# Performance work log

Hardware: AMD Instinct MI355X
Metric: run time of the kernel (lower is better)

Reference implementation:

```python
import jax, jax.numpy as jnp
import numpy as np

N = 524288
E = 16          # embedding_dim
R = 128         # dense grid resolution
H = 128         # hidden_dim
W0_SIREN = 30.0


def trilinear(grid, p):
    """grid: [R,R,R,E]; p: [N,3] in [0,1]. Returns [N,E]."""
    r = grid.shape[0]
    x = p * (r - 1)
    i0 = jnp.clip(jnp.floor(x), 0, r - 2).astype(jnp.int32)   # [N,3]
    f = x - i0.astype(x.dtype)                                # [N,3] fractional
    gf = grid.reshape(-1, grid.shape[-1])                     # [R^3, E]
    out = jnp.zeros((p.shape[0], grid.shape[-1]), dtype=grid.dtype)
    for dx in (0, 1):
        wx = f[:, 0] if dx else (1.0 - f[:, 0])
        for dy in (0, 1):
            wy = f[:, 1] if dy else (1.0 - f[:, 1])
            for dz in (0, 1):
                wz = f[:, 2] if dz else (1.0 - f[:, 2])
                idx = (i0[:, 0] + dx) * r * r + (i0[:, 1] + dy) * r + (i0[:, 2] + dz)
                out = out + gf[idx] * (wx * wy * wz)[:, None]
    return out


def siren(h, W0, b0, W1, b1, Wo, bo):
    h = jnp.sin(W0_SIREN * (h @ W0.T + b0))
    h = jnp.sin(W0_SIREN * (h @ W1.T + b1))
    return h @ Wo.T + bo   # [N,1]


def setup_inputs() -> dict:
    key = jax.random.key(0)
    ks = jax.random.split(key, 8)
    positions = jax.random.uniform(ks[0], (N, 3), dtype=jnp.float32)  # in [0,1)
    grid = jax.random.uniform(ks[1], (R, R, R, E), jnp.float32, -1e-4, 1e-4)
    din = E + 3
    c0 = float(np.sqrt(6.0 / din) / W0_SIREN)
    c1 = float(np.sqrt(6.0 / H) / W0_SIREN)
    W0 = jax.random.uniform(ks[2], (H, din), jnp.float32, -c0, c0)
    b0 = jax.random.uniform(ks[3], (H,), jnp.float32, -c0, c0)
    W1 = jax.random.uniform(ks[4], (H, H), jnp.float32, -c1, c1)
    b1 = jax.random.uniform(ks[5], (H,), jnp.float32, -c1, c1)
    Wo = jax.random.uniform(ks[6], (1, H), jnp.float32, -c1, c1)
    bo = jax.random.uniform(ks[7], (1,), jnp.float32, -c1, c1)
    return {"positions": positions, "grid": grid, "W0": W0, "b0": b0,
            "W1": W1, "b1": b1, "Wo": Wo, "bo": bo}


def reference(positions, grid, W0, b0, W1, b1, Wo, bo):
    # torch code rebinds positions = positions*0.5+0.5 BEFORE autograd.grad,
    # so the eikonal gradient is w.r.t. the transformed coordinates p.
    p = positions * 0.5 + 0.5

    def sdf_fn(pp):
        emb = trilinear(grid, pp)
        return siren(jnp.concatenate([emb, pp], axis=-1), W0, b0, W1, b1, Wo, bo)

    sdf, vjp_fn = jax.vjp(sdf_fn, p)
    (grad_x,) = vjp_fn(jnp.ones_like(sdf))
    return sdf, grad_x
```

## Files before the change

kernel.cpp:

```cpp
#include <hip/hip_runtime.h>
#include <math.h>

#define NPTS 524288
#define EDIM 16
#define RES  128
#define HDIM 128
#define DIN  19
#define OXs  (RES*RES*EDIM)
#define OYs  (RES*EDIM)
#define OZs  (EDIM)
#define NBLK 256
#define NWAVE 12
#define BATCH (NWAVE * 16)
#define NITER 11

typedef _Float16 f16;
typedef __attribute__((ext_vector_type(8))) _Float16 f16x8;
typedef __attribute__((ext_vector_type(4))) float f32x4;

#define WS_P1 0
#define WS_P2 32768
#define WS_P0 65536
#define WS_P3 73728
#define WS_T  81920
#define WS_BYTES 84992

__global__ void pack_weights(const float* __restrict__ W0, const float* __restrict__ b0,
                             const float* __restrict__ W1, const float* __restrict__ b1,
                             const float* __restrict__ Wo, unsigned char* __restrict__ ws) {
    int idx = blockIdx.x * 256 + threadIdx.x;
    f16* p1 = (f16*)(ws + WS_P1);
    f16* p2 = (f16*)(ws + WS_P2);
    f16* p0 = (f16*)(ws + WS_P0);
    f16* p3 = (f16*)(ws + WS_P3);
    float* tb = (float*)(ws + WS_T);
    if (idx < 16384) {
        int e = idx & 7, l = (idx >> 3) & 63, t = (idx >> 9) & 3, nt = idx >> 11;
        int c = l & 15, g = l >> 4;
        p1[idx] = (f16)W1[(c + 16*nt)*HDIM + (8*g + e + 32*t)];
    } else if (idx < 32768) {
        int i = idx - 16384;
        int e = i & 7, l = (i >> 3) & 63, t = (i >> 9) & 3, nt = i >> 11;
        int c = l & 15, g = l >> 4;
        p2[i] = (f16)W1[(8*g + e + 32*t)*HDIM + (c + 16*nt)];
    } else if (idx < 36864) {
        int i = idx - 32768;
        int e = i & 7, l = (i >> 3) & 63, nt = i >> 9;
        int c = l & 15, g = l >> 4;
        int d = 8*g + e;
        p0[i] = (d < EDIM) ? (f16)W0[(c + 16*nt)*DIN + d] : (f16)0.f;
    } else if (idx < 40960) {
        int i = idx - 36864;
        int e = i & 7, l = (i >> 3) & 63, t = (i >> 9) & 3, nt = i >> 11;
        int c = l & 15, g = l >> 4;
        int din = c + 16*nt;
        p3[i] = (din < DIN) ? (f16)W0[(8*g + e + 32*t)*DIN + din] : (f16)0.f;
    } else if (idx < 41728) {
        int i = idx - 40960;
        int j = i & 127, sel = i >> 7;
        float v;
        if (sel == 0)      v = W0[j*DIN + 16];
        else if (sel == 1) v = W0[j*DIN + 17];
        else if (sel == 2) v = W0[j*DIN + 18];
        else if (sel == 3) v = b0[j];
        else if (sel == 4) v = b1[j];
        else               v = Wo[j];
        tb[i] = v;
    }
}

__global__ __launch_bounds__(768, 1)
void sdf_mfma(const float* __restrict__ pos,
              const float* __restrict__ gridp,
              const unsigned char* __restrict__ ws,
              const float* __restrict__ bo,
              float* __restrict__ out) {
    __shared__ f16 sP1[16384];
    __shared__ f16 sP2[16384];
    __shared__ f16 sP0[4096];
    __shared__ f16 sP3[4096];
    __shared__ float sT[768];
    __shared__ unsigned char sBounce[NWAVE][4352];

    const int tid = threadIdx.x;
    {
        const uint4* src = (const uint4*)ws;
        uint4* d1 = (uint4*)sP1;
        uint4* d2 = (uint4*)sP2;
        uint4* d0 = (uint4*)sP0;
        uint4* d3 = (uint4*)sP3;
        uint4* dt = (uint4*)sT;
#pragma unroll
        for (int i = 0; i < 3; ++i) {
            int k = tid + i * 768;
            if (k < 2048) { d1[k] = src[k]; d2[k] = src[2048 + k]; }
        }
        if (tid < 512) { d0[tid] = src[4096 + tid]; d3[tid] = src[4608 + tid]; }
        if (tid < 192) dt[tid] = src[5120 + tid];
    }
    __syncthreads();

    const int l = tid & 63, w = tid >> 6;
    const int c = l & 15, g = l >> 4;

    f16* sBW = (f16*)sBounce[w];
    const f16x8* P0 = (const f16x8*)sP0;
    const f16x8* P1 = (const f16x8*)sP1;
    const f16x8* P2 = (const f16x8*)sP2;
    const f16x8* P3 = (const f16x8*)sP3;
    const f32x4 z4 = {0.f, 0.f, 0.f, 0.f};
    const float bov = bo[0];

#pragma unroll 1
    for (int it = 0; it < NITER; ++it) {
        const int pbase = (blockIdx.x * NITER + it) * BATCH + w * 16;
        if (pbase >= NPTS) continue;
        const int pt = pbase + c;

        const float px = fmaf(pos[3*pt+0], 0.5f, 0.5f);
        const float py = fmaf(pos[3*pt+1], 0.5f, 0.5f);
        const float pz = fmaf(pos[3*pt+2], 0.5f, 0.5f);
        const float x0 = px*127.f, x1 = py*127.f, x2 = pz*127.f;
        int i0 = (int)floorf(x0); i0 = i0 < 0 ? 0 : (i0 > 126 ? 126 : i0);
        int i1 = (int)floorf(x1); i1 = i1 < 0 ? 0 : (i1 > 126 ? 126 : i1);
        int i2 = (int)floorf(x2); i2 = i2 < 0 ? 0 : (i2 > 126 ? 126 : i2);
        const float f0 = x0 - (float)i0, f1 = x1 - (float)i1, f2 = x2 - (float)i2;
        const float wx1 = f0, wx0 = 1.f - f0;
        const float wy1 = f1, wy0 = 1.f - f1;
        const float wz1 = f2, wz0 = 1.f - f2;
        const float* gb = gridp + (size_t)((i0*RES + i1)*RES + i2)*EDIM;

        float w8[8] = {0.f,0.f,0.f,0.f,0.f,0.f,0.f,0.f};
        if (g < 2) {
#pragma unroll
            for (int cr = 0; cr < 8; ++cr) {
                const float* gp = gb + ((cr>>2)&1)*OXs + ((cr>>1)&1)*OYs + (cr&1)*OZs + 8*g;
                float4 qa = *(const float4*)gp;
                float4 qb = *(const float4*)(gp + 4);
                const float wc = ((cr&4)?wx1:wx0) * ((cr&2)?wy1:wy0) * ((cr&1)?wz1:wz0);
                w8[0] = fmaf(wc, qa.x, w8[0]);  w8[1] = fmaf(wc, qa.y, w8[1]);
                w8[2] = fmaf(wc, qa.z, w8[2]);  w8[3] = fmaf(wc, qa.w, w8[3]);
                w8[4] = fmaf(wc, qb.x, w8[4]);  w8[5] = fmaf(wc, qb.y, w8[5]);
                w8[6] = fmaf(wc, qb.z, w8[6]);  w8[7] = fmaf(wc, qb.w, w8[7]);
            }
        }
        f16x8 afe;
#pragma unroll
        for (int m = 0; m < 8; ++m) afe[m] = (f16)w8[m];

        f32x4 acc[8];
#pragma unroll
        for (int nt = 0; nt < 8; ++nt)
            acc[nt] = __builtin_amdgcn_mfma_f32_16x16x32_f16(afe, P0[nt*64 + l], z4, 0, 0, 0);

        float rpx[4], rpy[4], rpz[4];
#pragma unroll
        for (int r = 0; r < 4; ++r) {
            const int pr = pbase + 4*g + r;
            rpx[r] = fmaf(pos[3*pr+0], 0.5f, 0.5f);
            rpy[r] = fmaf(pos[3*pr+1], 0.5f, 0.5f);
            rpz[r] = fmaf(pos[3*pr+2], 0.5f, 0.5f);
        }
        float t0a[8][4];
#pragma unroll
        for (int nt = 0; nt < 8; ++nt) {
            const int j = c + 16*nt;
            const float t16 = sT[j], t17 = sT[128+j], t18 = sT[256+j], tb0 = sT[384+j];
#pragma unroll
            for (int r = 0; r < 4; ++r) {
                float a0 = acc[nt][r] + tb0;
                a0 = fmaf(rpx[r], t16, a0);
                a0 = fmaf(rpy[r], t17, a0);
                a0 = fmaf(rpz[r], t18, a0);
                const float t0 = 30.f * a0;
                t0a[nt][r] = t0;
                sBW[(4*g + r)*136 + j] = (f16)__sinf(t0);
            }
        }
        asm volatile("s_waitcnt lgkmcnt(0)" ::: "memory");

        f16x8 af[4];
#pragma unroll
        for (int t = 0; t < 4; ++t)
            af[t] = *(const f16x8*)&sBW[c*136 + 32*t + 8*g];
#pragma unroll
        for (int nt = 0; nt < 8; ++nt) {
            f32x4 a = z4;
#pragma unroll
            for (int t = 0; t < 4; ++t)
                a = __builtin_amdgcn_mfma_f32_16x16x32_f16(af[t], P1[(nt*4+t)*64 + l], a, 0, 0, 0);
            acc[nt] = a;
        }

        float sp[4] = {0.f, 0.f, 0.f, 0.f};
#pragma unroll
        for (int nt = 0; nt < 8; ++nt) {
            const int j = c + 16*nt;
            const float b1j = sT[512+j], woj = sT[640+j];
#pragma unroll
            for (int r = 0; r < 4; ++r) {
                const float t1 = 30.f * (acc[nt][r] + b1j);
                sp[r] = fmaf(woj, __sinf(t1), sp[r]);
                sBW[(4*g + r)*136 + j] = (f16)(30.f * woj * __cosf(t1));
            }
        }
#pragma unroll
        for (int r = 0; r < 4; ++r) {
            sp[r] += __shfl_xor(sp[r], 1);
            sp[r] += __shfl_xor(sp[r], 2);
            sp[r] += __shfl_xor(sp[r], 4);
            sp[r] += __shfl_xor(sp[r], 8);
        }
        if (c == 0) {
#pragma unroll
            for (int r = 0; r < 4; ++r) out[pbase + 4*g + r] = sp[r] + bov;
        }
        asm volatile("s_waitcnt lgkmcnt(0)" ::: "memory");

        float4 ca[2][4];
#pragma unroll
        for (int h = 0; h < 2; ++h) {
            const int cr = 2*g + h;
            const float* gp = gb + ((cr>>2)&1)*OXs + ((cr>>1)&1)*OYs + (cr&1)*OZs;
            ca[h][0] = *(const float4*)gp;
            ca[h][1] = *(const float4*)(gp + 4);
            ca[h][2] = *(const float4*)(gp + 8);
            ca[h][3] = *(const float4*)(gp + 12);
        }

#pragma unroll
        for (int t = 0; t < 4; ++t)
            af[t] = *(const f16x8*)&sBW[c*136 + 32*t + 8*g];
#pragma unroll
        for (int nt = 0; nt < 8; ++nt) {
            f32x4 a = z4;
#pragma unroll
            for (int t = 0; t < 4; ++t)
                a = __builtin_amdgcn_mfma_f32_16x16x32_f16(af[t], P2[(nt*4+t)*64 + l], a, 0, 0, 0);
            acc[nt] = a;
        }

#pragma unroll
        for (int nt = 0; nt < 8; ++nt) {
            const int k = c + 16*nt;
#pragma unroll
            for (int r = 0; r < 4; ++r) {
                const float da0 = acc[nt][r] * (30.f * __cosf(t0a[nt][r]));
                sBW[(4*g + r)*136 + k] = (f16)da0;
            }
        }
        asm volatile("s_waitcnt lgkmcnt(0)" ::: "memory");

#pragma unroll
        for (int t = 0; t < 4; ++t)
            af[t] = *(const f16x8*)&sBW[c*136 + 32*t + 8*g];
        f32x4 d3a = z4, d3b = z4;
#pragma unroll
        for (int t = 0; t < 4; ++t) {
            d3a = __builtin_amdgcn_mfma_f32_16x16x32_f16(af[t], P3[t*64 + l],     d3a, 0, 0, 0);
            d3b = __builtin_amdgcn_mfma_f32_16x16x32_f16(af[t], P3[(4+t)*64 + l], d3b, 0, 0, 0);
        }

        float* sDV = (float*)sBounce[w];
#pragma unroll
        for (int r = 0; r < 4; ++r) sDV[(4*g + r)*20 + c] = d3a[r];
        if (c < 3) {
#pragma unroll
            for (int r = 0; r < 4; ++r) sDV[(4*g + r)*20 + 16 + c] = d3b[r];
        }
        asm volatile("s_waitcnt lgkmcnt(0)" ::: "memory");

        const f32x4 dva = *(const f32x4*)&sDV[c*20 + 0];
        const f32x4 dvb = *(const f32x4*)&sDV[c*20 + 4];
        const f32x4 dvc = *(const f32x4*)&sDV[c*20 + 8];
        const f32x4 dvd = *(const f32x4*)&sDV[c*20 + 12];
        float scv[2];
#pragma unroll
        for (int h = 0; h < 2; ++h) {
            float s = ca[h][0].x*dva[0] + ca[h][0].y*dva[1] + ca[h][0].z*dva[2] + ca[h][0].w*dva[3]
                    + ca[h][1].x*dvb[0] + ca[h][1].y*dvb[1] + ca[h][1].z*dvb[2] + ca[h][1].w*dvb[3]
                    + ca[h][2].x*dvc[0] + ca[h][2].y*dvc[1] + ca[h][2].z*dvc[2] + ca[h][2].w*dvc[3]
                    + ca[h][3].x*dvd[0] + ca[h][3].y*dvd[1] + ca[h][3].z*dvd[2] + ca[h][3].w*dvd[3];
            scv[h] = s;
        }
        float* sSC = (float*)sBounce[w] + 320;
        sSC[c*8 + 2*g]     = scv[0];
        sSC[c*8 + 2*g + 1] = scv[1];
        asm volatile("s_waitcnt lgkmcnt(0)" ::: "memory");
        if (g == 0) {
            const float* scp = &sSC[c*8];
            const float sc0 = scp[0], sc1 = scp[1], sc2 = scp[2], sc3 = scp[3];
            const float sc4 = scp[4], sc5 = scp[5], sc6 = scp[6], sc7 = scp[7];
            const float gx = 127.f * (wy0*wz0*(sc4-sc0) + wy0*wz1*(sc5-sc1) +
                                      wy1*wz0*(sc6-sc2) + wy1*wz1*(sc7-sc3));
            const float gy = 127.f * (wx0*wz0*(sc2-sc0) + wx0*wz1*(sc3-sc1) +
                                      wx1*wz0*(sc6-sc4) + wx1*wz1*(sc7-sc5));
            const float gz = 127.f * (wx0*wy0*(sc1-sc0) + wx0*wy1*(sc3-sc2) +
                                      wx1*wy0*(sc5-sc4) + wx1*wy1*(sc7-sc6));
            out[NPTS + 3*pt + 0] = gx + sDV[c*20 + 16];
            out[NPTS + 3*pt + 1] = gy + sDV[c*20 + 17];
            out[NPTS + 3*pt + 2] = gz + sDV[c*20 + 18];
        }
    }
}

#define JCHUNK 64
__global__ void transpose_w1(const float* __restrict__ W1, float* __restrict__ W1T) {
    int idx = blockIdx.x * 256 + threadIdx.x;
    if (idx < HDIM * HDIM) {
        int j = idx >> 7, k = idx & 127;
        W1T[k * HDIM + j] = W1[j * HDIM + k];
    }
}
#define LOAD16(gq)                                   \
    float4 q0 = *(const float4*)((gq) + 0);          \
    float4 q1 = *(const float4*)((gq) + 4);          \
    float4 q2 = *(const float4*)((gq) + 8);          \
    float4 q3 = *(const float4*)((gq) + 12);

template<int RS, int CS>
__global__ __launch_bounds__(256, 2)
void sdf_fused(const float* __restrict__ pos, const float* __restrict__ gridp,
               const float* __restrict__ W0, const float* __restrict__ b0,
               const float* __restrict__ W1m, const float* __restrict__ b1,
               const float* __restrict__ Wo, const float* __restrict__ bo,
               float* __restrict__ out) {
    const int i = blockIdx.x * 256 + threadIdx.x;
    if (i >= NPTS) return;
    const float W0S = 30.0f;
    const float px = fmaf(pos[3*i+0], 0.5f, 0.5f);
    const float py = fmaf(pos[3*i+1], 0.5f, 0.5f);
    const float pz = fmaf(pos[3*i+2], 0.5f, 0.5f);
    const float x0 = px*127.f, x1 = py*127.f, x2 = pz*127.f;
    int i0 = (int)floorf(x0); i0 = i0 < 0 ? 0 : (i0 > 126 ? 126 : i0);
    int i1 = (int)floorf(x1); i1 = i1 < 0 ? 0 : (i1 > 126 ? 126 : i1);
    int i2 = (int)floorf(x2); i2 = i2 < 0 ? 0 : (i2 > 126 ? 126 : i2);
    const float f0 = x0-(float)i0, f1 = x1-(float)i1, f2 = x2-(float)i2;
    const float wx1 = f0, wx0 = 1.f-f0, wy1 = f1, wy0 = 1.f-f1, wz1 = f2, wz0 = 1.f-f2;
    const float* gb = gridp + (size_t)((i0*RES+i1)*RES+i2)*EDIM;
    float cw[8];
    cw[0]=wx0*wy0*wz0; cw[1]=wx0*wy0*wz1; cw[2]=wx0*wy1*wz0; cw[3]=wx0*wy1*wz1;
    cw[4]=wx1*wy0*wz0; cw[5]=wx1*wy0*wz1; cw[6]=wx1*wy1*wz0; cw[7]=wx1*wy1*wz1;
    float v[DIN];
#pragma unroll
    for (int e = 0; e < EDIM; ++e) v[e] = 0.f;
#pragma unroll
    for (int cr = 0; cr < 8; ++cr) {
        const float* gq = gb + ((cr>>2)&1)*OXs + ((cr>>1)&1)*OYs + (cr&1)*OZs;
        LOAD16(gq);
        const float wc = cw[cr];
        v[0]=fmaf(wc,q0.x,v[0]); v[1]=fmaf(wc,q0.y,v[1]); v[2]=fmaf(wc,q0.z,v[2]); v[3]=fmaf(wc,q0.w,v[3]);
        v[4]=fmaf(wc,q1.x,v[4]); v[5]=fmaf(wc,q1.y,v[5]); v[6]=fmaf(wc,q1.z,v[6]); v[7]=fmaf(wc,q1.w,v[7]);
        v[8]=fmaf(wc,q2.x,v[8]); v[9]=fmaf(wc,q2.y,v[9]); v[10]=fmaf(wc,q2.z,v[10]); v[11]=fmaf(wc,q2.w,v[11]);
        v[12]=fmaf(wc,q3.x,v[12]); v[13]=fmaf(wc,q3.y,v[13]); v[14]=fmaf(wc,q3.z,v[14]); v[15]=fmaf(wc,q3.w,v[15]);
    }
    v[16]=px; v[17]=py; v[18]=pz;
    float dv[DIN];
#pragma unroll
    for (int m = 0; m < DIN; ++m) dv[m] = 0.f;
    float sdf = bo[0];
#pragma unroll 1
    for (int cch = 0; cch < HDIM/JCHUNK; ++cch) {
        const int j0 = cch * JCHUNK;
        float a1c[JCHUNK];
#pragma unroll
        for (int jj = 0; jj < JCHUNK; ++jj) a1c[jj] = 0.f;
#pragma unroll 1
        for (int k = 0; k < HDIM; ++k) {
            float a0 = b0[k];
            const float* w0r = W0 + k*DIN;
#pragma unroll
            for (int m = 0; m < DIN; ++m) a0 = fmaf(w0r[m], v[m], a0);
            const float h1 = __sinf(W0S*a0);
            const float* wr = W1m + k*RS + j0*CS;
#pragma unroll
            for (int jj = 0; jj < JCHUNK; ++jj) a1c[jj] = fmaf(wr[jj*CS], h1, a1c[jj]);
        }
#pragma unroll
        for (int jj = 0; jj < JCHUNK; ++jj) {
            const float t = W0S*(a1c[jj] + b1[j0+jj]);
            float s, co; __sincosf(t, &s, &co);
            const float wo = Wo[j0+jj];
            sdf = fmaf(wo, s, sdf);
            a1c[jj] = (W0S*wo)*co;
        }
#pragma unroll 1
        for (int k = 0; k < HDIM; ++k) {
            const float* wr = W1m + k*RS + j0*CS;
            float s0=0.f,s1=0.f,s2=0.f,s3=0.f;
#pragma unroll
            for (int jj = 0; jj < JCHUNK; jj += 4) {
                s0 = fmaf(wr[(jj+0)*CS], a1c[jj+0], s0);
                s1 = fmaf(wr[(jj+1)*CS], a1c[jj+1], s1);
                s2 = fmaf(wr[(jj+2)*CS], a1c[jj+2], s2);
                s3 = fmaf(wr[(jj+3)*CS], a1c[jj+3], s3);
            }
            const float dh1 = (s0+s1)+(s2+s3);
            float a0 = b0[k];
            const float* w0r = W0 + k*DIN;
#pragma unroll
            for (int m = 0; m < DIN; ++m) a0 = fmaf(w0r[m], v[m], a0);
            const float da0 = dh1 * W0S * __cosf(W0S*a0);
#pragma unroll
            for (int m = 0; m < DIN; ++m) dv[m] = fmaf(w0r[m], da0, dv[m]);
        }
    }
    float sc[8];
#pragma unroll
    for (int cr = 0; cr < 8; ++cr) {
        const float* gq = gb + ((cr>>2)&1)*OXs + ((cr>>1)&1)*OYs + (cr&1)*OZs;
        LOAD16(gq);
        float t0 = q0.x*dv[0]+q0.y*dv[1]+q0.z*dv[2]+q0.w*dv[3];
        float t1 = q1.x*dv[4]+q1.y*dv[5]+q1.z*dv[6]+q1.w*dv[7];
        float t2 = q2.x*dv[8]+q2.y*dv[9]+q2.z*dv[10]+q2.w*dv[11];
        float t3 = q3.x*dv[12]+q3.y*dv[13]+q3.z*dv[14]+q3.w*dv[15];
        sc[cr] = (t0+t1)+(t2+t3);
    }
    const float gx = 127.f*(wy0*wz0*(sc[4]-sc[0]) + wy0*wz1*(sc[5]-sc[1]) + wy1*wz0*(sc[6]-sc[2]) + wy1*wz1*(sc[7]-sc[3]));
    const float gy = 127.f*(wx0*wz0*(sc[2]-sc[0]) + wx0*wz1*(sc[3]-sc[1]) + wx1*wz0*(sc[6]-sc[4]) + wx1*wz1*(sc[7]-sc[5]));
    const float gz = 127.f*(wx0*wy0*(sc[1]-sc[0]) + wx0*wy1*(sc[3]-sc[2]) + wx1*wy0*(sc[5]-sc[4]) + wx1*wy1*(sc[7]-sc[6]));
    out[i] = sdf;
    out[NPTS + 3*i + 0] = gx + dv[16];
    out[NPTS + 3*i + 1] = gy + dv[17];
    out[NPTS + 3*i + 2] = gz + dv[18];
}

extern "C" void kernel_launch(void* const* d_in, const int* in_sizes, int n_in,
                              void* d_out, int out_size, void* d_ws, size_t ws_size,
                              hipStream_t stream) {
    const float* pos  = (const float*)d_in[0];
    const float* grid = (const float*)d_in[1];
    const float* W0   = (const float*)d_in[2];
    const float* b0   = (const float*)d_in[3];
    const float* W1   = (const float*)d_in[4];
    const float* b1   = (const float*)d_in[5];
    const float* Wo   = (const float*)d_in[6];
    const float* bo   = (const float*)d_in[7];
    float* out = (float*)d_out;

    if (ws_size >= (size_t)WS_BYTES) {
        pack_weights<<<(41728 + 255)/256, 256, 0, stream>>>(W0, b0, W1, b1, Wo, (unsigned char*)d_ws);
        sdf_mfma<<<NBLK, 768, 0, stream>>>(pos, grid, (const unsigned char*)d_ws, bo, out);
    } else if (ws_size >= (size_t)(HDIM*HDIM*sizeof(float))) {
        float* W1T = (float*)d_ws;
        transpose_w1<<<(HDIM*HDIM + 255)/256, 256, 0, stream>>>(W1, W1T);
        sdf_fused<HDIM, 1><<<NPTS/256, 256, 0, stream>>>(pos, grid, W0, b0, W1T, b1, Wo, bo, out);
    } else {
        sdf_fused<1, HDIM><<<NPTS/256, 256, 0, stream>>>(pos, grid, W0, b0, W1, b1, Wo, bo, out);
    }
}
```

Baseline: 115.6 us.

## Hold small MFMA B operands in registers, split gather across lanes, raise MFMA priority

The P0 and P3 weight fragments now stay in VGPRs per wave instead of LDS, which removes LDS reads from the first and last matmuls and shrinks shared memory. The trilinear embedding gather is spread over all four lane groups: each handles one x-side of the cell and partial sums are combined with a cross-half shuffle, so the gather is no longer confined to half the wave. MFMA sections are wrapped in s_setprio to favour matrix issue across waves. These changes raise register pressure and add a shuffle, which could cause spills at 768 threads.

```diff
diff --git a/kernel.cpp b/kernel.cpp
--- a/kernel.cpp
+++ b/kernel.cpp
@@ -77,8 +77,6 @@
               float* __restrict__ out) {
     __shared__ f16 sP1[16384];
     __shared__ f16 sP2[16384];
-    __shared__ f16 sP0[4096];
-    __shared__ f16 sP3[4096];
     __shared__ float sT[768];
     __shared__ unsigned char sBounce[NWAVE][4352];
 
@@ -87,29 +85,35 @@
         const uint4* src = (const uint4*)ws;
         uint4* d1 = (uint4*)sP1;
         uint4* d2 = (uint4*)sP2;
-        uint4* d0 = (uint4*)sP0;
-        uint4* d3 = (uint4*)sP3;
         uint4* dt = (uint4*)sT;
 #pragma unroll
         for (int i = 0; i < 3; ++i) {
             int k = tid + i * 768;
             if (k < 2048) { d1[k] = src[k]; d2[k] = src[2048 + k]; }
         }
-        if (tid < 512) { d0[tid] = src[4096 + tid]; d3[tid] = src[4608 + tid]; }
         if (tid < 192) dt[tid] = src[5120 + tid];
     }
-    __syncthreads();
 
     const int l = tid & 63, w = tid >> 6;
     const int c = l & 15, g = l >> 4;
 
+    f16x8 B0r[8], B3r[8];
+    {
+        const f16x8* P0g = (const f16x8*)(ws + WS_P0);
+        const f16x8* P3g = (const f16x8*)(ws + WS_P3);
+#pragma unroll
+        for (int nt = 0; nt < 8; ++nt) B0r[nt] = P0g[nt*64 + l];
+#pragma unroll
+        for (int t = 0; t < 8; ++t)  B3r[t] = P3g[t*64 + l];
+    }
+    __syncthreads();
+
     f16* sBW = (f16*)sBounce[w];
-    const f16x8* P0 = (const f16x8*)sP0;
     const f16x8* P1 = (const f16x8*)sP1;
     const f16x8* P2 = (const f16x8*)sP2;
-    const f16x8* P3 = (const f16x8*)sP3;
     const f32x4 z4 = {0.f, 0.f, 0.f, 0.f};
     const float bov = bo[0];
+    const int s = g & 1, q = g >> 1;
 
 #pragma unroll 1
     for (int it = 0; it < NITER; ++it) {
@@ -131,13 +135,14 @@
         const float* gb = gridp + (size_t)((i0*RES + i1)*RES + i2)*EDIM;
 
         float w8[8] = {0.f,0.f,0.f,0.f,0.f,0.f,0.f,0.f};
-        if (g < 2) {
-#pragma unroll
-            for (int cr = 0; cr < 8; ++cr) {
-                const float* gp = gb + ((cr>>2)&1)*OXs + ((cr>>1)&1)*OYs + (cr&1)*OZs + 8*g;
+        {
+            const float wxq = q ? wx1 : wx0;
+#pragma unroll
+            for (int j = 0; j < 4; ++j) {
+                const float* gp = gb + q*OXs + ((j>>1)&1)*OYs + (j&1)*OZs + 8*s;
                 float4 qa = *(const float4*)gp;
                 float4 qb = *(const float4*)(gp + 4);
-                const float wc = ((cr&4)?wx1:wx0) * ((cr&2)?wy1:wy0) * ((cr&1)?wz1:wz0);
+                const float wc = wxq * ((j&2)?wy1:wy0) * ((j&1)?wz1:wz0);
                 w8[0] = fmaf(wc, qa.x, w8[0]);  w8[1] = fmaf(wc, qa.y, w8[1]);
                 w8[2] = fmaf(wc, qa.z, w8[2]);  w8[3] = fmaf(wc, qa.w, w8[3]);
                 w8[4] = fmaf(wc, qb.x, w8[4]);  w8[5] = fmaf(wc, qb.y, w8[5]);
@@ -146,12 +151,17 @@
         }
         f16x8 afe;
 #pragma unroll
-        for (int m = 0; m < 8; ++m) afe[m] = (f16)w8[m];
+        for (int m = 0; m < 8; ++m) {
+            const float full = w8[m] + __shfl_xor(w8[m], 32);
+            afe[m] = (g < 2) ? (f16)full : (f16)0.f;
+        }
 
         f32x4 acc[8];
+        __builtin_amdgcn_s_setprio(1);
 #pragma unroll
         for (int nt = 0; nt < 8; ++nt)
-            acc[nt] = __builtin_amdgcn_mfma_f32_16x16x32_f16(afe, P0[nt*64 + l], z4, 0, 0, 0);
+            acc[nt] = __builtin_amdgcn_mfma_f32_16x16x32_f16(afe, B0r[nt], z4, 0, 0, 0);
+        __builtin_amdgcn_s_setprio(0);
 
         float rpx[4], rpy[4], rpz[4];
 #pragma unroll
@@ -183,6 +193,7 @@
 #pragma unroll
         for (int t = 0; t < 4; ++t)
             af[t] = *(const f16x8*)&sBW[c*136 + 32*t + 8*g];
+        __builtin_amdgcn_s_setprio(1);
 #pragma unroll
         for (int nt = 0; nt < 8; ++nt) {
             f32x4 a = z4;
@@ -191,6 +202,7 @@
                 a = __builtin_amdgcn_mfma_f32_16x16x32_f16(af[t], P1[(nt*4+t)*64 + l], a, 0, 0, 0);
             acc[nt] = a;
         }
+        __builtin_amdgcn_s_setprio(0);
 
         float sp[4] = {0.f, 0.f, 0.f, 0.f};
 #pragma unroll
@@ -231,6 +243,7 @@
 #pragma unroll
         for (int t = 0; t < 4; ++t)
             af[t] = *(const f16x8*)&sBW[c*136 + 32*t + 8*g];
+        __builtin_amdgcn_s_setprio(1);
 #pragma unroll
         for (int nt = 0; nt < 8; ++nt) {
             f32x4 a = z4;
@@ -239,6 +252,7 @@
                 a = __builtin_amdgcn_mfma_f32_16x16x32_f16(af[t], P2[(nt*4+t)*64 + l], a, 0, 0, 0);
             acc[nt] = a;
         }
+        __builtin_amdgcn_s_setprio(0);
 
 #pragma unroll
         for (int nt = 0; nt < 8; ++nt) {
@@ -255,11 +269,13 @@
         for (int t = 0; t < 4; ++t)
             af[t] = *(const f16x8*)&sBW[c*136 + 32*t + 8*g];
         f32x4 d3a = z4, d3b = z4;
+        __builtin_amdgcn_s_setprio(1);
 #pragma unroll
         for (int t = 0; t < 4; ++t) {
-            d3a = __builtin_amdgcn_mfma_f32_16x16x32_f16(af[t], P3[t*64 + l],     d3a, 0, 0, 0);
-            d3b = __builtin_amdgcn_mfma_f32_16x16x32_f16(af[t], P3[(4+t)*64 + l], d3b, 0, 0, 0);
-        }
+            d3a = __builtin_amdgcn_mfma_f32_16x16x32_f16(af[t], B3r[t],     d3a, 0, 0, 0);
+            d3b = __builtin_amdgcn_mfma_f32_16x16x32_f16(af[t], B3r[4 + t], d3b, 0, 0, 0);
+        }
+        __builtin_amdgcn_s_setprio(0);
 
         float* sDV = (float*)sBounce[w];
 #pragma unroll
@@ -277,11 +293,11 @@
         float scv[2];
 #pragma unroll
         for (int h = 0; h < 2; ++h) {
-            float s = ca[h][0].x*dva[0] + ca[h][0].y*dva[1] + ca[h][0].z*dva[2] + ca[h][0].w*dva[3]
-                    + ca[h][1].x*dvb[0] + ca[h][1].y*dvb[1] + ca[h][1].z*dvb[2] + ca[h][1].w*dvb[3]
-                    + ca[h][2].x*dvc[0] + ca[h][2].y*dvc[1] + ca[h][2].z*dvc[2] + ca[h][2].w*dvc[3]
-                    + ca[h][3].x*dvd[0] + ca[h][3].y*dvd[1] + ca[h][3].z*dvd[2] + ca[h][3].w*dvd[3];
-            scv[h] = s;
+            float sdot = ca[h][0].x*dva[0] + ca[h][0].y*dva[1] + ca[h][0].z*dva[2] + ca[h][0].w*dva[3]
+                       + ca[h][1].x*dvb[0] + ca[h][1].y*dvb[1] + ca[h][1].z*dvb[2] + ca[h][1].w*dvb[3]
+                       + ca[h][2].x*dvc[0] + ca[h][2].y*dvc[1] + ca[h][2].z*dvc[2] + ca[h][2].w*dvc[3]
+                       + ca[h][3].x*dvd[0] + ca[h][3].y*dvd[1] + ca[h][3].z*dvd[2] + ca[h][3].w*dvd[3];
+            scv[h] = sdot;
         }
         float* sSC = (float*)sBounce[w] + 320;
         sSC[c*8 + 2*g]     = scv[0];
@@ -379,9 +395,9 @@
 #pragma unroll
         for (int jj = 0; jj < JCHUNK; ++jj) {
             const float t = W0S*(a1c[jj] + b1[j0+jj]);
-            float s, co; __sincosf(t, &s, &co);
+            float sv, co; __sincosf(t, &sv, &co);
             const float wo = Wo[j0+jj];
-            sdf = fmaf(wo, s, sdf);
+            sdf = fmaf(wo, sv, sdf);
             a1c[jj] = (W0S*wo)*co;
         }
 #pragma unroll 1
```

Measured after the change: 194.2 us. +68.1%, slower.
